# Kernel tuning notes

Hardware: AMD Instinct MI355X
Metric: run time of the kernel (lower is better)

The kernel has to match this reference:

```python
import jax, jax.numpy as jnp
import numpy as np

ALPHA, BETA, GAMMA = 0.5, 0.003, 0.001
NUM_CLASSES = 1000
NUM_FEATURES = 1000
BATCH = 16384


def setup_inputs() -> dict:
    key = jax.random.key(0)
    k1, k2, k3 = jax.random.split(key, 3)
    x = jax.random.normal(k1, (BATCH, NUM_FEATURES), dtype=jnp.float32)
    y = jax.random.randint(k2, (BATCH,), 0, NUM_CLASSES)
    centers = jax.random.normal(k3, (NUM_CLASSES, NUM_FEATURES), dtype=jnp.float32)
    return {"x": x, "y": y, "centers": centers}


def reference(x, y, centers):
    B = x.shape[0]
    C = NUM_CLASSES
    # cross entropy (x used as logits, as in nn.CrossEntropyLoss)
    logp = jax.nn.log_softmax(x, axis=-1)
    ce = -jnp.mean(jnp.take_along_axis(logp, y[:, None], axis=1))
    # center loss on PRE-update centers
    c_y = centers[y]                       # [B, F]
    delta = x - c_y
    center_loss = jnp.mean(jnp.sum(delta * delta, axis=1))
    # functional form of the in-place per-class center update:
    # centers[i] += alpha * mean(delta[y == i])
    counts = jax.ops.segment_sum(jnp.ones((B,), x.dtype), y, num_segments=C)  # [C]
    sum_delta = jax.ops.segment_sum(delta, y, num_segments=C)                 # [C, F]
    mean_delta = jnp.where(counts[:, None] > 0,
                           sum_delta / jnp.maximum(counts, 1)[:, None],
                           jnp.zeros_like(sum_delta))
    new_centers = centers + ALPHA * mean_delta
    # inter loss: sum_{i<j} ||c_i - c_j||^2 = C*sum_i||c_i||^2 - ||sum_i c_i||^2
    sq = jnp.sum(new_centers * new_centers, axis=1)   # [C]
    s = jnp.sum(new_centers, axis=0)                  # [F]
    num_pairs = C * (C - 1) / 2
    inter_loss = (C * jnp.sum(sq) - jnp.sum(s * s)) / num_pairs
    # intra loss on POST-update centers: mean over class, averaged over classes
    d2 = jnp.sum((x - new_centers[y]) ** 2, axis=1)   # [B]
    per_class_sum = jax.ops.segment_sum(d2, y, num_segments=C)
    per_class_mean = jnp.where(counts > 0, per_class_sum / jnp.maximum(counts, 1),
                               jnp.zeros_like(per_class_sum))
    intra_loss = jnp.sum(per_class_mean) / C
    return ce + BETA * center_loss + GAMMA * inter_loss + GAMMA * intra_loss
```

## Files before the change

### kernel.cpp

```cpp
#include <hip/hip_runtime.h>
#include <math.h>

#define NF 1000
#define NC 1000
#define NB 16384
#define NV 250
#define ALPHA_C 0.5f
#define BETA_C 0.003f
#define GAMMA_C 0.001f
#define MAXL 512

__device__ __forceinline__ float wave_sum(float v) {
#pragma unroll
    for (int off = 32; off > 0; off >>= 1) v += __shfl_xor(v, off, 64);
    return v;
}
__device__ __forceinline__ float wave_max(float v) {
#pragma unroll
    for (int off = 32; off > 0; off >>= 1) v = fmaxf(v, __shfl_xor(v, off, 64));
    return v;
}

__global__ __launch_bounds__(256) void class_fused(
    const float* __restrict__ x, const int* __restrict__ y,
    const float* __restrict__ centers,
    float* __restrict__ new_centers, float4* __restrict__ partials) {
    __shared__ int list[MAXL];
    __shared__ int lcount;
    __shared__ float sb[24];
    __shared__ float sxy[2];
    const int c = blockIdx.x, t = threadIdx.x;
    const int wid = t >> 6, lane = t & 63;
    if (t == 0) lcount = 0;
    __syncthreads();

    const int4* y4 = (const int4*)y;
    for (int i = t; i < NB / 4; i += 256) {
        int4 v = y4[i];
        int b = 4 * i;
        if (v.x == c) { int p = atomicAdd(&lcount, 1); list[p & (MAXL - 1)] = b; }
        if (v.y == c) { int p = atomicAdd(&lcount, 1); list[p & (MAXL - 1)] = b + 1; }
        if (v.z == c) { int p = atomicAdd(&lcount, 1); list[p & (MAXL - 1)] = b + 2; }
        if (v.w == c) { int p = atomicAdd(&lcount, 1); list[p & (MAXL - 1)] = b + 3; }
    }
    __syncthreads();
    const int n = lcount;

    float4 cv = make_float4(0.f, 0.f, 0.f, 0.f);
    if (t < NV) cv = ((const float4*)(centers + (size_t)c * NF))[t];
    const int xt = c >> 2, xc = c & 3;

    float4 acc = make_float4(0.f, 0.f, 0.f, 0.f);
    float ce_acc = 0.f, s2_acc = 0.f;

    for (int i = 0; i < n; i += 2) {
        const bool two = (i + 1 < n);
        const int b0 = list[i];
        const int b1 = two ? list[i + 1] : 0;
        float4 v0, v1;
        float m0 = -INFINITY, m1 = -INFINITY;
        if (t < NV) {
            v0 = ((const float4*)(x + (size_t)b0 * NF))[t];
            m0 = fmaxf(fmaxf(v0.x, v0.y), fmaxf(v0.z, v0.w));
            if (two) {
                v1 = ((const float4*)(x + (size_t)b1 * NF))[t];
                m1 = fmaxf(fmaxf(v1.x, v1.y), fmaxf(v1.z, v1.w));
            }
        }
        m0 = wave_max(m0);
        m1 = wave_max(m1);
        __syncthreads();
        if (lane == 0) { sb[wid] = m0; sb[4 + wid] = m1; }
        if (t == xt) {
            sxy[0] = (xc == 0) ? v0.x : (xc == 1) ? v0.y : (xc == 2) ? v0.z : v0.w;
            if (two) sxy[1] = (xc == 0) ? v1.x : (xc == 1) ? v1.y : (xc == 2) ? v1.z : v1.w;
        }
        __syncthreads();
        const float rmax0 = fmaxf(fmaxf(sb[0], sb[1]), fmaxf(sb[2], sb[3]));
        const float rmax1 = fmaxf(fmaxf(sb[4], sb[5]), fmaxf(sb[6], sb[7]));

        float e0 = 0.f, e1 = 0.f, d0 = 0.f, d1 = 0.f;
        if (t < NV) {
            e0 = expf(v0.x - rmax0) + expf(v0.y - rmax0) +
                 expf(v0.z - rmax0) + expf(v0.w - rmax0);
            float dx = v0.x - cv.x, dy = v0.y - cv.y;
            float dz = v0.z - cv.z, dw = v0.w - cv.w;
            d0 = dx * dx + dy * dy + dz * dz + dw * dw;
            acc.x += v0.x; acc.y += v0.y; acc.z += v0.z; acc.w += v0.w;
            if (two) {
                e1 = expf(v1.x - rmax1) + expf(v1.y - rmax1) +
                     expf(v1.z - rmax1) + expf(v1.w - rmax1);
                float ex = v1.x - cv.x, ey = v1.y - cv.y;
                float ez = v1.z - cv.z, ew = v1.w - cv.w;
                d1 = ex * ex + ey * ey + ez * ez + ew * ew;
                acc.x += v1.x; acc.y += v1.y; acc.z += v1.z; acc.w += v1.w;
            }
        }
        e0 = wave_sum(e0); e1 = wave_sum(e1);
        d0 = wave_sum(d0); d1 = wave_sum(d1);
        if (lane == 0) { sb[8 + wid] = e0; sb[12 + wid] = e1;
                         sb[16 + wid] = d0; sb[20 + wid] = d1; }
        __syncthreads();
        if (t == 0) {
            float se0 = sb[8] + sb[9] + sb[10] + sb[11];
            float sd0 = sb[16] + sb[17] + sb[18] + sb[19];
            ce_acc += -(sxy[0] - rmax0 - logf(se0));
            s2_acc += sd0;
            if (two) {
                float se1 = sb[12] + sb[13] + sb[14] + sb[15];
                float sd1 = sb[20] + sb[21] + sb[22] + sb[23];
                ce_acc += -(sxy[1] - rmax1 - logf(se1));
                s2_acc += sd1;
            }
        }
    }

    const float inv = (n > 0) ? 1.f / (float)n : 0.f;
    float lsq = 0.f, lmd2 = 0.f;
    if (t < NV) {
        float4 md, nc;
        md.x = (n > 0) ? (acc.x * inv - cv.x) : 0.f;
        md.y = (n > 0) ? (acc.y * inv - cv.y) : 0.f;
        md.z = (n > 0) ? (acc.z * inv - cv.z) : 0.f;
        md.w = (n > 0) ? (acc.w * inv - cv.w) : 0.f;
        nc.x = cv.x + ALPHA_C * md.x; nc.y = cv.y + ALPHA_C * md.y;
        nc.z = cv.z + ALPHA_C * md.z; nc.w = cv.w + ALPHA_C * md.w;
        ((float4*)(new_centers + (size_t)c * NF))[t] = nc;
        lsq = nc.x * nc.x + nc.y * nc.y + nc.z * nc.z + nc.w * nc.w;
        lmd2 = md.x * md.x + md.y * md.y + md.z * md.z + md.w * md.w;
    }
    float w0 = wave_sum(lsq), w1 = wave_sum(lmd2);
    __syncthreads();
    if (lane == 0) { sb[wid] = w0; sb[4 + wid] = w1; }
    __syncthreads();
    if (t == 0) {
        float sq = sb[0] + sb[1] + sb[2] + sb[3];
        float md2 = sb[4] + sb[5] + sb[6] + sb[7];
        float intra = (n > 0) ? (s2_acc * inv - ALPHA_C * (2.f - ALPHA_C) * md2) : 0.f;
        partials[c] = make_float4(ce_acc, s2_acc, sq, intra);
    }
}

__global__ __launch_bounds__(256) void col_partial(
    const float* __restrict__ new_centers, float* __restrict__ s_part) {
    const int f = blockIdx.x * 256 + threadIdx.x;
    if (f >= NF) return;
    float acc = 0.f;
    for (int c = blockIdx.y; c < NC; c += gridDim.y)
        acc += new_centers[(size_t)c * NF + f];
    s_part[blockIdx.y * NF + f] = acc;
}

__global__ __launch_bounds__(1024) void finalize(
    const float* __restrict__ s_part, const float4* __restrict__ partials,
    float* __restrict__ out) {
    __shared__ float sb[80];
    const int t = threadIdx.x;
    float ssq = 0.f, ces = 0.f, s2 = 0.f, sq = 0.f, intra = 0.f;
    if (t < NC) {
        float s = 0.f;
#pragma unroll
        for (int k = 0; k < 16; k++) s += s_part[k * NF + t];
        ssq = s * s;
        float4 p = partials[t];
        ces = p.x; s2 = p.y; sq = p.z; intra = p.w;
    }
    float w0 = wave_sum(ssq), w1 = wave_sum(ces), w2 = wave_sum(s2);
    float w3 = wave_sum(sq), w4 = wave_sum(intra);
    const int wid = t >> 6, lane = t & 63;
    if (lane == 0) {
        sb[wid] = w0; sb[16 + wid] = w1; sb[32 + wid] = w2;
        sb[48 + wid] = w3; sb[64 + wid] = w4;
    }
    __syncthreads();
    if (t == 0) {
        float Sssq = 0.f, Sces = 0.f, Ss2 = 0.f, Ssq = 0.f, Sintra = 0.f;
        for (int k = 0; k < 16; k++) {
            Sssq += sb[k]; Sces += sb[16 + k]; Ss2 += sb[32 + k];
            Ssq += sb[48 + k]; Sintra += sb[64 + k];
        }
        float cem = Sces / (float)NB;
        float cl = Ss2 / (float)NB;
        float num_pairs = (float)NC * (float)(NC - 1) * 0.5f;
        float inter = ((float)NC * Ssq - Sssq) / num_pairs;
        float intra_l = Sintra / (float)NC;
        out[0] = cem + BETA_C * cl + GAMMA_C * inter + GAMMA_C * intra_l;
    }
}

extern "C" void kernel_launch(void* const* d_in, const int* in_sizes, int n_in,
                              void* d_out, int out_size, void* d_ws, size_t ws_size,
                              hipStream_t stream) {
    const float* x = (const float*)d_in[0];
    const int* y = (const int*)d_in[1];
    const float* centers = (const float*)d_in[2];
    float* out = (float*)d_out;

    char* ws = (char*)d_ws;
    float* s_part      = (float*)(ws);
    float4* partials   = (float4*)(ws + 64000);
    float* new_centers = (float*)(ws + 80000);

    class_fused<<<NC, 256, 0, stream>>>(x, y, centers, new_centers, partials);
    dim3 cgrid(4, 16);
    col_partial<<<cgrid, 256, 0, stream>>>(new_centers, s_part);
    finalize<<<1, 1024, 0, stream>>>(s_part, partials, out);
}
```

Baseline: 140.8 us.

## Process one sample row per wavefront to remove block-wide syncs per row

Each of the four wavefronts now handles its own rows, two at a time with a stride of eight, holding the full 1000-float row in registers across four float4 slots per lane. Max, sum-exp and squared distance are reduced with wave shuffles only, and the target logit is fetched with a lane shuffle. This removes the three __syncthreads and the shared-memory scratch per pair of rows, and lets independent waves overlap their loads. Per-wave class accumulators are then merged serially through shared memory, which uses more registers and adds a short reduction epilogue.

```diff
diff --git a/kernel.cpp b/kernel.cpp
--- a/kernel.cpp
+++ b/kernel.cpp
@@ -21,14 +21,46 @@
     return v;
 }
 
+__device__ __forceinline__ void do_row(
+    const float4* __restrict__ v, const float4* __restrict__ cvv,
+    float4* __restrict__ acc, int lane, int j_src, int lane_src, int comp,
+    float& ce_acc, float& s2_acc) {
+    float m = -INFINITY;
+#pragma unroll
+    for (int j = 0; j < 4; j++)
+        m = fmaxf(m, fmaxf(fmaxf(v[j].x, v[j].y), fmaxf(v[j].z, v[j].w)));
+    const float rmax = wave_max(m);
+    float e = 0.f, d = 0.f;
+#pragma unroll
+    for (int j = 0; j < 4; j++) {
+        const int idx = lane + 64 * j;
+        e += expf(v[j].x - rmax) + expf(v[j].y - rmax) +
+             expf(v[j].z - rmax) + expf(v[j].w - rmax);
+        if (idx < NV) {
+            float dx = v[j].x - cvv[j].x, dy = v[j].y - cvv[j].y;
+            float dz = v[j].z - cvv[j].z, dw = v[j].w - cvv[j].w;
+            d += dx * dx + dy * dy + dz * dz + dw * dw;
+            acc[j].x += v[j].x; acc[j].y += v[j].y;
+            acc[j].z += v[j].z; acc[j].w += v[j].w;
+        }
+    }
+    const float se = wave_sum(e);
+    const float sd = wave_sum(d);
+    float4 xj = (j_src == 0) ? v[0] : (j_src == 1) ? v[1] : (j_src == 2) ? v[2] : v[3];
+    float cand = (comp == 0) ? xj.x : (comp == 1) ? xj.y : (comp == 2) ? xj.z : xj.w;
+    const float xy = __shfl(cand, lane_src, 64);
+    ce_acc += -(xy - rmax - logf(se));
+    s2_acc += sd;
+}
+
 __global__ __launch_bounds__(256) void class_fused(
     const float* __restrict__ x, const int* __restrict__ y,
     const float* __restrict__ centers,
     float* __restrict__ new_centers, float4* __restrict__ partials) {
     __shared__ int list[MAXL];
     __shared__ int lcount;
-    __shared__ float sb[24];
-    __shared__ float sxy[2];
+    __shared__ float4 smx[NV];
+    __shared__ float sb[8];
     const int c = blockIdx.x, t = threadIdx.x;
     const int wid = t >> 6, lane = t & 63;
     if (t == 0) lcount = 0;
@@ -46,98 +78,91 @@
     __syncthreads();
     const int n = lcount;
 
-    float4 cv = make_float4(0.f, 0.f, 0.f, 0.f);
-    if (t < NV) cv = ((const float4*)(centers + (size_t)c * NF))[t];
-    const int xt = c >> 2, xc = c & 3;
-
-    float4 acc = make_float4(0.f, 0.f, 0.f, 0.f);
+    float4 cvv[4];
+    const float4* crow = (const float4*)(centers + (size_t)c * NF);
+#pragma unroll
+    for (int j = 0; j < 4; j++) {
+        const int idx = lane + 64 * j;
+        cvv[j] = (idx < NV) ? crow[idx] : make_float4(0.f, 0.f, 0.f, 0.f);
+    }
+
+    const int f4 = c >> 2;
+    const int j_src = f4 >> 6, lane_src = f4 & 63, comp = c & 3;
+
+    float4 acc[4];
+#pragma unroll
+    for (int j = 0; j < 4; j++) acc[j] = make_float4(0.f, 0.f, 0.f, 0.f);
     float ce_acc = 0.f, s2_acc = 0.f;
 
-    for (int i = 0; i < n; i += 2) {
-        const bool two = (i + 1 < n);
-        const int b0 = list[i];
-        const int b1 = two ? list[i + 1] : 0;
-        float4 v0, v1;
-        float m0 = -INFINITY, m1 = -INFINITY;
-        if (t < NV) {
-            v0 = ((const float4*)(x + (size_t)b0 * NF))[t];
-            m0 = fmaxf(fmaxf(v0.x, v0.y), fmaxf(v0.z, v0.w));
-            if (two) {
-                v1 = ((const float4*)(x + (size_t)b1 * NF))[t];
-                m1 = fmaxf(fmaxf(v1.x, v1.y), fmaxf(v1.z, v1.w));
+    for (int i = wid; i < n; i += 8) {
+        const int ib = i + 4;
+        const bool hb = (ib < n);
+        const float4* ra = (const float4*)(x + (size_t)list[i] * NF);
+        const float4* rb = (const float4*)(x + (size_t)(hb ? list[ib] : list[i]) * NF);
+        float4 va[4], vb[4];
+#pragma unroll
+        for (int j = 0; j < 4; j++) {
+            const int idx = lane + 64 * j;
+            if (idx < NV) { va[j] = ra[idx]; vb[j] = rb[idx]; }
+            else {
+                va[j] = make_float4(-INFINITY, -INFINITY, -INFINITY, -INFINITY);
+                vb[j] = va[j];
             }
         }
-        m0 = wave_max(m0);
-        m1 = wave_max(m1);
+        do_row(va, cvv, acc, lane, j_src, lane_src, comp, ce_acc, s2_acc);
+        if (hb) do_row(vb, cvv, acc, lane, j_src, lane_src, comp, ce_acc, s2_acc);
+    }
+
+    for (int w = 0; w < 4; w++) {
+        if (wid == w) {
+#pragma unroll
+            for (int j = 0; j < 4; j++) {
+                const int idx = lane + 64 * j;
+                if (idx < NV) {
+                    if (w == 0) smx[idx] = acc[j];
+                    else {
+                        float4 s = smx[idx];
+                        s.x += acc[j].x; s.y += acc[j].y;
+                        s.z += acc[j].z; s.w += acc[j].w;
+                        smx[idx] = s;
+                    }
+                }
+            }
+        }
         __syncthreads();
-        if (lane == 0) { sb[wid] = m0; sb[4 + wid] = m1; }
-        if (t == xt) {
-            sxy[0] = (xc == 0) ? v0.x : (xc == 1) ? v0.y : (xc == 2) ? v0.z : v0.w;
-            if (two) sxy[1] = (xc == 0) ? v1.x : (xc == 1) ? v1.y : (xc == 2) ? v1.z : v1.w;
-        }
-        __syncthreads();
-        const float rmax0 = fmaxf(fmaxf(sb[0], sb[1]), fmaxf(sb[2], sb[3]));
-        const float rmax1 = fmaxf(fmaxf(sb[4], sb[5]), fmaxf(sb[6], sb[7]));
-
-        float e0 = 0.f, e1 = 0.f, d0 = 0.f, d1 = 0.f;
-        if (t < NV) {
-            e0 = expf(v0.x - rmax0) + expf(v0.y - rmax0) +
-                 expf(v0.z - rmax0) + expf(v0.w - rmax0);
-            float dx = v0.x - cv.x, dy = v0.y - cv.y;
-            float dz = v0.z - cv.z, dw = v0.w - cv.w;
-            d0 = dx * dx + dy * dy + dz * dz + dw * dw;
-            acc.x += v0.x; acc.y += v0.y; acc.z += v0.z; acc.w += v0.w;
-            if (two) {
-                e1 = expf(v1.x - rmax1) + expf(v1.y - rmax1) +
-                     expf(v1.z - rmax1) + expf(v1.w - rmax1);
-                float ex = v1.x - cv.x, ey = v1.y - cv.y;
-                float ez = v1.z - cv.z, ew = v1.w - cv.w;
-                d1 = ex * ex + ey * ey + ez * ez + ew * ew;
-                acc.x += v1.x; acc.y += v1.y; acc.z += v1.z; acc.w += v1.w;
+    }
+    if (lane == 0) { sb[wid] = ce_acc; sb[4 + wid] = s2_acc; }
+    __syncthreads();
+
+    if (wid == 0) {
+        const float inv = (n > 0) ? 1.f / (float)n : 0.f;
+        float lsq = 0.f, lmd2 = 0.f;
+        float4* ncrow = (float4*)(new_centers + (size_t)c * NF);
+#pragma unroll
+        for (int j = 0; j < 4; j++) {
+            const int idx = lane + 64 * j;
+            if (idx < NV) {
+                float4 s = smx[idx];
+                float4 md, nc;
+                md.x = (n > 0) ? (s.x * inv - cvv[j].x) : 0.f;
+                md.y = (n > 0) ? (s.y * inv - cvv[j].y) : 0.f;
+                md.z = (n > 0) ? (s.z * inv - cvv[j].z) : 0.f;
+                md.w = (n > 0) ? (s.w * inv - cvv[j].w) : 0.f;
+                nc.x = cvv[j].x + ALPHA_C * md.x; nc.y = cvv[j].y + ALPHA_C * md.y;
+                nc.z = cvv[j].z + ALPHA_C * md.z; nc.w = cvv[j].w + ALPHA_C * md.w;
+                ncrow[idx] = nc;
+                lsq  += nc.x * nc.x + nc.y * nc.y + nc.z * nc.z + nc.w * nc.w;
+                lmd2 += md.x * md.x + md.y * md.y + md.z * md.z + md.w * md.w;
             }
         }
-        e0 = wave_sum(e0); e1 = wave_sum(e1);
-        d0 = wave_sum(d0); d1 = wave_sum(d1);
-        if (lane == 0) { sb[8 + wid] = e0; sb[12 + wid] = e1;
-                         sb[16 + wid] = d0; sb[20 + wid] = d1; }
-        __syncthreads();
-        if (t == 0) {
-            float se0 = sb[8] + sb[9] + sb[10] + sb[11];
-            float sd0 = sb[16] + sb[17] + sb[18] + sb[19];
-            ce_acc += -(sxy[0] - rmax0 - logf(se0));
-            s2_acc += sd0;
-            if (two) {
-                float se1 = sb[12] + sb[13] + sb[14] + sb[15];
-                float sd1 = sb[20] + sb[21] + sb[22] + sb[23];
-                ce_acc += -(sxy[1] - rmax1 - logf(se1));
-                s2_acc += sd1;
-            }
-        }
-    }
-
-    const float inv = (n > 0) ? 1.f / (float)n : 0.f;
-    float lsq = 0.f, lmd2 = 0.f;
-    if (t < NV) {
-        float4 md, nc;
-        md.x = (n > 0) ? (acc.x * inv - cv.x) : 0.f;
-        md.y = (n > 0) ? (acc.y * inv - cv.y) : 0.f;
-        md.z = (n > 0) ? (acc.z * inv - cv.z) : 0.f;
-        md.w = (n > 0) ? (acc.w * inv - cv.w) : 0.f;
-        nc.x = cv.x + ALPHA_C * md.x; nc.y = cv.y + ALPHA_C * md.y;
-        nc.z = cv.z + ALPHA_C * md.z; nc.w = cv.w + ALPHA_C * md.w;
-        ((float4*)(new_centers + (size_t)c * NF))[t] = nc;
-        lsq = nc.x * nc.x + nc.y * nc.y + nc.z * nc.z + nc.w * nc.w;
-        lmd2 = md.x * md.x + md.y * md.y + md.z * md.z + md.w * md.w;
-    }
-    float w0 = wave_sum(lsq), w1 = wave_sum(lmd2);
-    __syncthreads();
-    if (lane == 0) { sb[wid] = w0; sb[4 + wid] = w1; }
-    __syncthreads();
-    if (t == 0) {
-        float sq = sb[0] + sb[1] + sb[2] + sb[3];
-        float md2 = sb[4] + sb[5] + sb[6] + sb[7];
-        float intra = (n > 0) ? (s2_acc * inv - ALPHA_C * (2.f - ALPHA_C) * md2) : 0.f;
-        partials[c] = make_float4(ce_acc, s2_acc, sq, intra);
+        const float sq = wave_sum(lsq);
+        const float md2 = wave_sum(lmd2);
+        if (lane == 0) {
+            const float ces = sb[0] + sb[1] + sb[2] + sb[3];
+            const float s2 = sb[4] + sb[5] + sb[6] + sb[7];
+            const float intra = (n > 0) ? (s2 * inv - ALPHA_C * (2.f - ALPHA_C) * md2) : 0.f;
+            partials[c] = make_float4(ces, s2, sq, intra);
+        }
     }
 }
 
```

New measurement: 161.9 us. 1.15x slower.
